# Kernel optimization log

Measured on AMD Instinct MI355X. Metric: run time of the kernel, lower is better.

The kernel has to match this reference:

```python
import jax, jax.numpy as jnp
import numpy as np

B, S, E = 2, 2048, 1024
H, HKV = 16, 4
D = E // H          # head_dim = 64
REP = H // HKV      # kv repeat factor = 4


def setup_inputs() -> dict:
    key = jax.random.key(0)
    ks = jax.random.split(key, 9)
    std = 0.02
    x = jax.random.normal(ks[0], (B, S, E), dtype=jnp.float32)
    # causal mask: True means masked (upper triangle, strictly above diagonal)
    mask = jnp.triu(jnp.ones((S, S), dtype=bool), k=1)
    wq_w = jax.random.normal(ks[1], (E, E), dtype=jnp.float32) * std
    wq_b = jax.random.normal(ks[2], (E,), dtype=jnp.float32) * std
    wk_w = jax.random.normal(ks[3], (HKV * D, E), dtype=jnp.float32) * std
    wk_b = jax.random.normal(ks[4], (HKV * D,), dtype=jnp.float32) * std
    wv_w = jax.random.normal(ks[5], (HKV * D, E), dtype=jnp.float32) * std
    wv_b = jax.random.normal(ks[6], (HKV * D,), dtype=jnp.float32) * std
    wo_w = jax.random.normal(ks[7], (E, E), dtype=jnp.float32) * std
    wo_b = jax.random.normal(ks[8], (E,), dtype=jnp.float32) * std
    return {"x": x, "mask": mask, "wq_w": wq_w, "wq_b": wq_b,
            "wk_w": wk_w, "wk_b": wk_b, "wv_w": wv_w, "wv_b": wv_b,
            "wo_w": wo_w, "wo_b": wo_b}


def reference(x, mask, wq_w, wq_b, wk_w, wk_b, wv_w, wv_b, wo_w, wo_b):
    b, s, e = x.shape
    # projections (torch Linear: x @ W.T + b)
    q = x @ wq_w.T + wq_b                       # [B,S,E]
    k = x @ wk_w.T + wk_b                       # [B,S,HKV*D]
    v = x @ wv_w.T + wv_b
    # q grouped by kv head: [B, HKV, REP, S, D]; k/v: [B, HKV, S, D]
    q = q.reshape(b, s, HKV, REP, D).transpose(0, 2, 3, 1, 4)
    k = k.reshape(b, s, HKV, D).transpose(0, 2, 1, 3)
    v = v.reshape(b, s, HKV, D).transpose(0, 2, 1, 3)
    scale = D ** (-0.5)
    # scores [B, HKV, REP, Sq, Skv] -- same math as physical repeat_kv
    scores = jnp.einsum('bgrsd,bgtd->bgrst', q, k) * scale
    scores = jnp.where(mask, -jnp.inf, scores)
    w = jax.nn.softmax(scores, axis=-1)
    ctx = jnp.einsum('bgrst,bgtd->bgrsd', w, v)  # [B,HKV,REP,S,D]
    ctx = ctx.transpose(0, 3, 1, 2, 4).reshape(b, s, e)
    return ctx @ wo_w.T + wo_b
```

## Files before the change

kernel.cpp:

```cpp
#include <hip/hip_runtime.h>


typedef __attribute__((ext_vector_type(8))) short bh8;
typedef __attribute__((ext_vector_type(4))) short sh4;
typedef __attribute__((ext_vector_type(4))) float fv4;
typedef __attribute__((ext_vector_type(2))) unsigned int uv2;

#define MFMA16 __builtin_amdgcn_mfma_f32_16x16x32_bf16

static __device__ __forceinline__ float fast_exp2(float x) {
  return __builtin_amdgcn_exp2f(x);
}
static __device__ __forceinline__ unsigned short f2bf(float f) {
  unsigned int u; __builtin_memcpy(&u, &f, 4);
  u += 0x7fffu + ((u >> 16) & 1u);
  return (unsigned short)(u >> 16);
}
static __device__ __forceinline__ unsigned int pack2(float a, float b) {
  return (unsigned int)(unsigned short)f2bf(a) |
         ((unsigned int)(unsigned short)f2bf(b) << 16);
}
static __device__ __forceinline__ void gload16(const short* g, short* l) {
  __builtin_amdgcn_global_load_lds(
      (const __attribute__((address_space(1))) void*)g,
      (__attribute__((address_space(3))) void*)l, 16, 0, 0);
}

static __device__ __forceinline__ bh8 pshuf(const float* p, int quad, int l16) {
  unsigned int u01 = pack2(p[0], p[1]);
  unsigned int u23 = pack2(p[2], p[3]);
  unsigned int u45 = pack2(p[4], p[5]);
  unsigned int u67 = pack2(p[6], p[7]);
  const int g0 = (((quad << 1)    ) & 3) * 16 + l16;
  const int g1 = (((quad << 1) + 1) & 3) * 16 + l16;
  unsigned int w0l = __shfl((int)u01, g0), w0h = __shfl((int)u45, g0);
  unsigned int w1l = __shfl((int)u23, g0), w1h = __shfl((int)u67, g0);
  unsigned int w2l = __shfl((int)u01, g1), w2h = __shfl((int)u45, g1);
  unsigned int w3l = __shfl((int)u23, g1), w3h = __shfl((int)u67, g1);
  const bool up = (quad & 2) != 0;
  union { unsigned int w[4]; bh8 v; } pu;
  pu.w[0] = up ? w0h : w0l;
  pu.w[1] = up ? w1h : w1l;
  pu.w[2] = up ? w2h : w2l;
  pu.w[3] = up ? w3h : w3l;
  return pu.v;
}

__global__ __launch_bounds__(256) void cvt_all(
    const float* __restrict__ x,  const float* __restrict__ wq,
    const float* __restrict__ wk, const float* __restrict__ wv,
    const float* __restrict__ wo,
    short* __restrict__ xb, short* __restrict__ wqkvb, short* __restrict__ wob)
{
  const int i = blockIdx.x * 256 + threadIdx.x;
  const float* src; short* dst; int j;
  if (i < 1048576)      { j = i;           src = x;  dst = xb; }
  else if (i < 1310720) { j = i - 1048576; src = wq; dst = wqkvb; }
  else if (i < 1376256) { j = i - 1310720; src = wk; dst = wqkvb + (size_t)1024 * 1024; }
  else if (i < 1441792) { j = i - 1376256; src = wv; dst = wqkvb + (size_t)1280 * 1024; }
  else                  { j = i - 1441792; src = wo; dst = wob; }
  const float4 v = ((const float4*)src)[j];
  sh4 o = { (short)f2bf(v.x), (short)f2bf(v.y),
            (short)f2bf(v.z), (short)f2bf(v.w) };
  ((sh4*)dst)[j] = o;
}

__global__ __launch_bounds__(256) void gemm_dbuf(
    const short* __restrict__ A, const short* __restrict__ W,
    const float* __restrict__ biasQ, const float* __restrict__ biasK,
    const float* __restrict__ biasV,
    short* __restrict__ Cq, short* __restrict__ Ck, short* __restrict__ Cvt,
    float* __restrict__ Cf,
    int M, int K, int S, int mode, float scaleQ)
{
  __shared__ short As[2][128 * 32];
  __shared__ short Bs[2][64 * 32];
  const int tid  = threadIdx.x;
  const int wave = tid >> 6, lane = tid & 63;
  const int quad = lane >> 4, l16 = lane & 15;
  const int row0 = blockIdx.x * 128, col0 = blockIdx.y * 64;
  const int wr = (wave >> 1) * 64, wc = (wave & 1) * 32;

  fv4 acc[4][2] = {};

  const int srow = wave * 16 + (lane >> 2);
  const int skp  = (lane & 3) * 8;
  const short* ag = A + (size_t)(row0 + srow) * K + skp;
  const short* bg = W + (size_t)(col0 + srow) * K + skp;

  auto stage = [&](int b, int k0) {
    gload16(ag + k0,                  &As[b][(wave * 16) * 32]);
    gload16(ag + (size_t)64 * K + k0, &As[b][(64 + wave * 16) * 32]);
    gload16(bg + k0,                  &Bs[b][(wave * 16) * 32]);
  };

  stage(0, 0);
  __syncthreads();
  const int nIter = K / 32;
  for (int it = 0; it < nIter; it++) {
    const int cur = it & 1;
    if (it + 1 < nIter) stage(cur ^ 1, (it + 1) * 32);

    bh8 af[4], bf[2];
    #pragma unroll
    for (int i = 0; i < 4; i++)
      af[i] = *(const bh8*)&As[cur][(wr + i * 16 + l16) * 32 + quad * 8];
    #pragma unroll
    for (int j = 0; j < 2; j++)
      bf[j] = *(const bh8*)&Bs[cur][(wc + j * 16 + l16) * 32 + quad * 8];
    #pragma unroll
    for (int i = 0; i < 4; i++)
      #pragma unroll
      for (int j = 0; j < 2; j++)
        acc[i][j] = MFMA16(af[i], bf[j], acc[i][j], 0, 0, 0);
    __syncthreads();
  }

  if (mode == 2) {
    float bv[2];
    #pragma unroll
    for (int j = 0; j < 2; j++) bv[j] = biasQ[col0 + wc + j * 16 + l16];
    #pragma unroll
    for (int i = 0; i < 4; i++) {
      const int row = row0 + wr + i * 16 + quad * 4;
      #pragma unroll
      for (int j = 0; j < 2; j++) {
        const int col = col0 + wc + j * 16 + l16;
        #pragma unroll
        for (int r = 0; r < 4; r++)
          Cf[(size_t)(row + r) * 1024 + col] = acc[i][j][r] + bv[j];
      }
    }
  } else if (col0 < 1024) {
    float bv[2];
    #pragma unroll
    for (int j = 0; j < 2; j++) bv[j] = biasQ[col0 + wc + j * 16 + l16];
    #pragma unroll
    for (int i = 0; i < 4; i++) {
      const int row = row0 + wr + i * 16 + quad * 4;
      #pragma unroll
      for (int j = 0; j < 2; j++) {
        const int col = col0 + wc + j * 16 + l16;
        #pragma unroll
        for (int r = 0; r < 4; r++)
          Cq[(size_t)(row + r) * 1024 + col] =
              (short)f2bf((acc[i][j][r] + bv[j]) * scaleQ);
      }
    }
  } else if (col0 < 1280) {
    float bv[2];
    #pragma unroll
    for (int j = 0; j < 2; j++) bv[j] = biasK[col0 + wc + j * 16 + l16 - 1024];
    #pragma unroll
    for (int i = 0; i < 4; i++) {
      const int row = row0 + wr + i * 16 + quad * 4;
      #pragma unroll
      for (int j = 0; j < 2; j++) {
        const int col = col0 + wc + j * 16 + l16 - 1024;
        #pragma unroll
        for (int r = 0; r < 4; r++)
          Ck[(size_t)(row + r) * 256 + col] = (short)f2bf(acc[i][j][r] + bv[j]);
      }
    }
  } else {
    float bv[2];
    #pragma unroll
    for (int j = 0; j < 2; j++) bv[j] = biasV[col0 + wc + j * 16 + l16 - 1280];
    const int b  = row0 / S;
    const int sb = row0 - b * S;
    #pragma unroll
    for (int i = 0; i < 4; i++) {
      const int s = sb + wr + i * 16 + quad * 4;
      #pragma unroll
      for (int j = 0; j < 2; j++) {
        const int np = col0 + wc + j * 16 + l16 - 1280;
        sh4 v = { (short)f2bf(acc[i][j][0] + bv[j]),
                  (short)f2bf(acc[i][j][1] + bv[j]),
                  (short)f2bf(acc[i][j][2] + bv[j]),
                  (short)f2bf(acc[i][j][3] + bv[j]) };
        *(sh4*)(Cvt + ((size_t)(b * 256 + np)) * S + s) = v;
      }
    }
  }
}

__global__ __launch_bounds__(256) void gqa_attn(
    const short* __restrict__ Q,
    const short* __restrict__ Kg,
    const short* __restrict__ Vt,
    short* __restrict__ ctx)
{
  const int S = 2048, E = 1024, KVE = 256;
  __shared__ short Ks[2][4096];
  __shared__ short Vs[2][4096];
  __shared__ short P2[4][16 * 72];

  const int wave = threadIdx.x >> 6;
  const int lane = threadIdx.x & 63;
  const int quad = lane >> 4, l16 = lane & 15;
  const int bh = blockIdx.y;
  const int b = bh >> 4, h = bh & 15, kv = h >> 2;

  const short* Kb = Kg + (size_t)b * S * KVE + kv * 64;
  const short* Vb = Vt + ((size_t)(b * 4 + kv)) * 64 * S;
  short* Pw = &P2[wave][0];

  const int srow = lane >> 3;
  const int scg  = (lane & 7) ^ srow;

  const int kc0 = (quad ^ (l16 & 7)) * 8;
  const int kc1 = ((quad ^ 4) ^ (l16 & 7)) * 8;
  const int pwr = l16 * 72;

  auto stageKV = [&](int buf, int t0) {
    #pragma unroll
    for (int e = 0; e < 2; e++) {
      const int g = wave * 2 + e;
      const int row = g * 8 + srow;
      gload16(Kb + (size_t)(t0 + row) * KVE + scg * 8, &Ks[buf][g * 512]);
      gload16(Vb + (size_t)row * S + t0 + scg * 8,     &Vs[buf][g * 512]);
    }
  };

  for (int ph = 0; ph < 2; ph++) {
    const int j = ph ? (31 - (int)blockIdx.x) : (int)blockIdx.x;
    const int qblk0 = j * 64;
    const int q0 = qblk0 + wave * 16;

    const short* qrow = Q + (size_t)(b * S + q0 + l16) * E + h * 64 + quad * 8;
    bh8 qf0 = *(const bh8*)(qrow);
    bh8 qf1 = *(const bh8*)(qrow + 32);

    fv4 acc0{}, acc1{}, acc2{}, acc3{};
    float rs = 0.f;

    const int nInt = qblk0 >> 6;
    if (nInt > 0) {
      stageKV(0, 0);
      __syncthreads();
      for (int it = 0; it < nInt; it++) {
        const int cur = it & 1;
        if (it + 1 < nInt) stageKV(cur ^ 1, (it + 1) * 64);

        fv4 st[4] = {};
        #pragma unroll
        for (int i = 0; i < 4; i++) {
          const int tb = (i * 16 + l16) * 64;
          bh8 k0 = *(const bh8*)&Ks[cur][tb + kc0];
          bh8 k1 = *(const bh8*)&Ks[cur][tb + kc1];
          st[i] = MFMA16(k0, qf0, st[i], 0, 0, 0);
          st[i] = MFMA16(k1, qf1, st[i], 0, 0, 0);
        }
        #pragma unroll
        for (int i = 0; i < 4; i++) {
          float p0 = fast_exp2(st[i][0]);
          float p1 = fast_exp2(st[i][1]);
          float p2 = fast_exp2(st[i][2]);
          float p3 = fast_exp2(st[i][3]);
          rs += (p0 + p1) + (p2 + p3);
          uv2 u = { pack2(p0, p1), pack2(p2, p3) };
          *(uv2*)&Pw[pwr + i * 16 + quad * 4] = u;
        }
        bh8 pfA = *(const bh8*)&Pw[pwr + quad * 8];
        bh8 pfB = *(const bh8*)&Pw[pwr + 32 + quad * 8];
        #pragma unroll
        for (int dt = 0; dt < 4; dt++) {
          const int db = (dt * 16 + l16) * 64;
          bh8 v0 = *(const bh8*)&Vs[cur][db + kc0];
          bh8 v1 = *(const bh8*)&Vs[cur][db + kc1];
          fv4* a = dt == 0 ? &acc0 : dt == 1 ? &acc1 : dt == 2 ? &acc2 : &acc3;
          *a = MFMA16(v0, pfA, *a, 0, 0, 0);
          *a = MFMA16(v1, pfB, *a, 0, 0, 0);
        }
        __syncthreads();
      }
    }

    const int nk = q0 + 16;
    for (int t0 = qblk0; t0 < nk; t0 += 32) {
      fv4 st0{}, st1{};
      {
        const short* kr = Kb + (size_t)(t0 + l16) * KVE + quad * 8;
        bh8 k0 = *(const bh8*)(kr);
        bh8 k1 = *(const bh8*)(kr + 32);
        st0 = MFMA16(k0, qf0, st0, 0, 0, 0);
        st0 = MFMA16(k1, qf1, st0, 0, 0, 0);
      }
      const bool do2 = (t0 + 16) < nk;
      if (do2) {
        const short* kr = Kb + (size_t)(t0 + 16 + l16) * KVE + quad * 8;
        bh8 k0 = *(const bh8*)(kr);
        bh8 k1 = *(const bh8*)(kr + 32);
        st1 = MFMA16(k0, qf0, st1, 0, 0, 0);
        st1 = MFMA16(k1, qf1, st1, 0, 0, 0);
      }
      const int qg = q0 + l16;
      float p[8];
      #pragma unroll
      for (int r = 0; r < 4; r++) {
        const int t = t0 + quad * 4 + r;
        p[r]     = (t <= qg)               ? fast_exp2(st0[r]) : 0.f;
        p[4 + r] = (do2 && (t + 16) <= qg) ? fast_exp2(st1[r]) : 0.f;
      }
      #pragma unroll
      for (int i = 0; i < 8; i++) rs += p[i];

      bh8 pf = pshuf(p, quad, l16);
      const short* vr = Vb + (size_t)l16 * S + t0 + quad * 8;
      acc0 = MFMA16(*(const bh8*)(vr),          pf, acc0, 0, 0, 0);
      acc1 = MFMA16(*(const bh8*)(vr + 16 * S), pf, acc1, 0, 0, 0);
      acc2 = MFMA16(*(const bh8*)(vr + 32 * S), pf, acc2, 0, 0, 0);
      acc3 = MFMA16(*(const bh8*)(vr + 48 * S), pf, acc3, 0, 0, 0);
    }

    float lsum = rs;
    lsum += __shfl_xor(lsum, 16);
    lsum += __shfl_xor(lsum, 32);
    const float inv = 1.f / lsum;

    short* orow = ctx + (size_t)(b * S + q0 + l16) * E + h * 64 + quad * 4;
    sh4 o0 = { (short)f2bf(acc0[0] * inv), (short)f2bf(acc0[1] * inv),
               (short)f2bf(acc0[2] * inv), (short)f2bf(acc0[3] * inv) };
    sh4 o1 = { (short)f2bf(acc1[0] * inv), (short)f2bf(acc1[1] * inv),
               (short)f2bf(acc1[2] * inv), (short)f2bf(acc1[3] * inv) };
    sh4 o2 = { (short)f2bf(acc2[0] * inv), (short)f2bf(acc2[1] * inv),
               (short)f2bf(acc2[2] * inv), (short)f2bf(acc2[3] * inv) };
    sh4 o3 = { (short)f2bf(acc3[0] * inv), (short)f2bf(acc3[1] * inv),
               (short)f2bf(acc3[2] * inv), (short)f2bf(acc3[3] * inv) };
    *(sh4*)(orow)      = o0;
    *(sh4*)(orow + 16) = o1;
    *(sh4*)(orow + 32) = o2;
    *(sh4*)(orow + 48) = o3;
  }
}

extern "C" void kernel_launch(void* const* d_in, const int* in_sizes, int n_in,
                              void* d_out, int out_size, void* d_ws, size_t ws_size,
                              hipStream_t stream)
{
  const float* x    = (const float*)d_in[0];
  const float* wq_w = (const float*)d_in[2];
  const float* wq_b = (const float*)d_in[3];
  const float* wk_w = (const float*)d_in[4];
  const float* wk_b = (const float*)d_in[5];
  const float* wv_w = (const float*)d_in[6];
  const float* wv_b = (const float*)d_in[7];
  const float* wo_w = (const float*)d_in[8];
  const float* wo_b = (const float*)d_in[9];
  float* out = (float*)d_out;

  const int S = 2048, E = 1024, M = 2 * S;
  const float sl2e = 0.125f * 1.44269504f;

  char* ob = (char*)d_out;
  short* Qb   = (short*)(ob);
  short* Kbuf = (short*)(ob + (size_t)( 8 << 20));
  short* Vtb  = (short*)(ob + (size_t)(10 << 20));

  char* ws = (char*)d_ws;
  short* xb    = (short*)(ws);
  short* wqkvb = (short*)(ws + (size_t)( 8 << 20));
  short* wob   = (short*)(ws + (size_t)(11 << 20));
  short* Cx    = xb;

  dim3 blk(256);
  cvt_all<<<dim3(6656), blk, 0, stream>>>(x, wq_w, wk_w, wv_w, wo_w,
                                          xb, wqkvb, wob);
  gemm_dbuf<<<dim3(M / 128, 1536 / 64), blk, 0, stream>>>(
      xb, wqkvb, wq_b, wk_b, wv_b, Qb, Kbuf, Vtb, nullptr, M, E, S, 0, sl2e);
  gqa_attn<<<dim3(16, 2 * 16), blk, 0, stream>>>(Qb, Kbuf, Vtb, Cx);
  gemm_dbuf<<<dim3(M / 128, 1024 / 64), blk, 0, stream>>>(
      Cx, wob, wo_b, nullptr, nullptr, nullptr, nullptr, nullptr, out,
      M, E, S, 2, 1.f);
}
```

Measured before the change: 181.0 us.

## Enlarge GEMM tiles to 128x128, split attention blocks, shuffle P in registers

The GEMM now uses 128x128 output tiles with a K-step of 64 and XOR-swizzled LDS in a single buffer. This raises data reuse per block but drops the double-buffered prefetch. The attention kernel no longer pairs a short and a long query block inside one workgroup; it launches one block per query tile with longest tiles first. The P matrix now goes to the PV MFMA through a register shuffle (pshuf) instead of a round trip through LDS. The trade-off is fewer GEMM blocks (more tail imbalance) and load latency that the single LDS buffer leaves exposed.

```diff
diff --git a/kernel.cpp b/kernel.cpp
--- a/kernel.cpp
+++ b/kernel.cpp
@@ -4,7 +4,6 @@
 typedef __attribute__((ext_vector_type(8))) short bh8;
 typedef __attribute__((ext_vector_type(4))) short sh4;
 typedef __attribute__((ext_vector_type(4))) float fv4;
-typedef __attribute__((ext_vector_type(2))) unsigned int uv2;
 
 #define MFMA16 __builtin_amdgcn_mfma_f32_16x16x32_bf16
 
@@ -65,7 +64,7 @@
   ((sh4*)dst)[j] = o;
 }
 
-__global__ __launch_bounds__(256) void gemm_dbuf(
+__global__ __launch_bounds__(256) void gemm_m97(
     const short* __restrict__ A, const short* __restrict__ W,
     const float* __restrict__ biasQ, const float* __restrict__ biasK,
     const float* __restrict__ biasV,
@@ -73,58 +72,58 @@
     float* __restrict__ Cf,
     int M, int K, int S, int mode, float scaleQ)
 {
-  __shared__ short As[2][128 * 32];
-  __shared__ short Bs[2][64 * 32];
-  const int tid  = threadIdx.x;
+  __shared__ short As[128 * 64];
+  __shared__ short Bs[128 * 64];
+  const int tid = threadIdx.x;
   const int wave = tid >> 6, lane = tid & 63;
   const int quad = lane >> 4, l16 = lane & 15;
-  const int row0 = blockIdx.x * 128, col0 = blockIdx.y * 64;
-  const int wr = (wave >> 1) * 64, wc = (wave & 1) * 32;
-
-  fv4 acc[4][2] = {};
-
-  const int srow = wave * 16 + (lane >> 2);
-  const int skp  = (lane & 3) * 8;
-  const short* ag = A + (size_t)(row0 + srow) * K + skp;
-  const short* bg = W + (size_t)(col0 + srow) * K + skp;
-
-  auto stage = [&](int b, int k0) {
-    gload16(ag + k0,                  &As[b][(wave * 16) * 32]);
-    gload16(ag + (size_t)64 * K + k0, &As[b][(64 + wave * 16) * 32]);
-    gload16(bg + k0,                  &Bs[b][(wave * 16) * 32]);
-  };
-
-  stage(0, 0);
-  __syncthreads();
-  const int nIter = K / 32;
-  for (int it = 0; it < nIter; it++) {
-    const int cur = it & 1;
-    if (it + 1 < nIter) stage(cur ^ 1, (it + 1) * 32);
-
-    bh8 af[4], bf[2];
-    #pragma unroll
-    for (int i = 0; i < 4; i++)
-      af[i] = *(const bh8*)&As[cur][(wr + i * 16 + l16) * 32 + quad * 8];
-    #pragma unroll
-    for (int j = 0; j < 2; j++)
-      bf[j] = *(const bh8*)&Bs[cur][(wc + j * 16 + l16) * 32 + quad * 8];
-    #pragma unroll
-    for (int i = 0; i < 4; i++)
-      #pragma unroll
-      for (int j = 0; j < 2; j++)
-        acc[i][j] = MFMA16(af[i], bf[j], acc[i][j], 0, 0, 0);
+  const int row0 = blockIdx.x * 128, col0 = blockIdx.y * 128;
+  const int wr = (wave >> 1) * 64, wc = (wave & 1) * 64;
+
+  fv4 acc[4][4] = {};
+
+  const int srow8  = lane >> 3;
+  const int schunk = (lane & 7) ^ srow8;
+  const short* agB = A + (size_t)(row0 + wave * 32 + srow8) * K + schunk * 8;
+  const short* bgB = W + (size_t)(col0 + wave * 32 + srow8) * K + schunk * 8;
+
+  const int fsw = (l16 & 7);
+
+  for (int k0 = 0; k0 < K; k0 += 64) {
     __syncthreads();
+    #pragma unroll
+    for (int g = 0; g < 4; g++) {
+      gload16(agB + (size_t)(g * 8) * K + k0, &As[(wave * 32 + g * 8) * 64]);
+      gload16(bgB + (size_t)(g * 8) * K + k0, &Bs[(wave * 32 + g * 8) * 64]);
+    }
+    __syncthreads();
+    #pragma unroll
+    for (int ks = 0; ks < 2; ks++) {
+      const int co = ((ks * 4 + quad) ^ fsw) * 8;
+      bh8 af[4], bf[4];
+      #pragma unroll
+      for (int i = 0; i < 4; i++)
+        af[i] = *(const bh8*)&As[(wr + i * 16 + l16) * 64 + co];
+      #pragma unroll
+      for (int j = 0; j < 4; j++)
+        bf[j] = *(const bh8*)&Bs[(wc + j * 16 + l16) * 64 + co];
+      #pragma unroll
+      for (int i = 0; i < 4; i++)
+        #pragma unroll
+        for (int j = 0; j < 4; j++)
+          acc[i][j] = MFMA16(af[i], bf[j], acc[i][j], 0, 0, 0);
+    }
   }
 
   if (mode == 2) {
-    float bv[2];
-    #pragma unroll
-    for (int j = 0; j < 2; j++) bv[j] = biasQ[col0 + wc + j * 16 + l16];
+    float bv[4];
+    #pragma unroll
+    for (int j = 0; j < 4; j++) bv[j] = biasQ[col0 + wc + j * 16 + l16];
     #pragma unroll
     for (int i = 0; i < 4; i++) {
       const int row = row0 + wr + i * 16 + quad * 4;
       #pragma unroll
-      for (int j = 0; j < 2; j++) {
+      for (int j = 0; j < 4; j++) {
         const int col = col0 + wc + j * 16 + l16;
         #pragma unroll
         for (int r = 0; r < 4; r++)
@@ -132,14 +131,14 @@
       }
     }
   } else if (col0 < 1024) {
-    float bv[2];
-    #pragma unroll
-    for (int j = 0; j < 2; j++) bv[j] = biasQ[col0 + wc + j * 16 + l16];
+    float bv[4];
+    #pragma unroll
+    for (int j = 0; j < 4; j++) bv[j] = biasQ[col0 + wc + j * 16 + l16];
     #pragma unroll
     for (int i = 0; i < 4; i++) {
       const int row = row0 + wr + i * 16 + quad * 4;
       #pragma unroll
-      for (int j = 0; j < 2; j++) {
+      for (int j = 0; j < 4; j++) {
         const int col = col0 + wc + j * 16 + l16;
         #pragma unroll
         for (int r = 0; r < 4; r++)
@@ -148,14 +147,14 @@
       }
     }
   } else if (col0 < 1280) {
-    float bv[2];
-    #pragma unroll
-    for (int j = 0; j < 2; j++) bv[j] = biasK[col0 + wc + j * 16 + l16 - 1024];
+    float bv[4];
+    #pragma unroll
+    for (int j = 0; j < 4; j++) bv[j] = biasK[col0 + wc + j * 16 + l16 - 1024];
     #pragma unroll
     for (int i = 0; i < 4; i++) {
       const int row = row0 + wr + i * 16 + quad * 4;
       #pragma unroll
-      for (int j = 0; j < 2; j++) {
+      for (int j = 0; j < 4; j++) {
         const int col = col0 + wc + j * 16 + l16 - 1024;
         #pragma unroll
         for (int r = 0; r < 4; r++)
@@ -163,16 +162,16 @@
       }
     }
   } else {
-    float bv[2];
-    #pragma unroll
-    for (int j = 0; j < 2; j++) bv[j] = biasV[col0 + wc + j * 16 + l16 - 1280];
+    float bv[4];
+    #pragma unroll
+    for (int j = 0; j < 4; j++) bv[j] = biasV[col0 + wc + j * 16 + l16 - 1280];
     const int b  = row0 / S;
     const int sb = row0 - b * S;
     #pragma unroll
     for (int i = 0; i < 4; i++) {
       const int s = sb + wr + i * 16 + quad * 4;
       #pragma unroll
-      for (int j = 0; j < 2; j++) {
+      for (int j = 0; j < 4; j++) {
         const int np = col0 + wc + j * 16 + l16 - 1280;
         sh4 v = { (short)f2bf(acc[i][j][0] + bv[j]),
                   (short)f2bf(acc[i][j][1] + bv[j]),
@@ -193,24 +192,23 @@
   const int S = 2048, E = 1024, KVE = 256;
   __shared__ short Ks[2][4096];
   __shared__ short Vs[2][4096];
-  __shared__ short P2[4][16 * 72];
 
   const int wave = threadIdx.x >> 6;
   const int lane = threadIdx.x & 63;
   const int quad = lane >> 4, l16 = lane & 15;
   const int bh = blockIdx.y;
   const int b = bh >> 4, h = bh & 15, kv = h >> 2;
+  const int j = 31 - (int)blockIdx.x;
+  const int qblk0 = j * 64;
+  const int q0 = qblk0 + wave * 16;
 
   const short* Kb = Kg + (size_t)b * S * KVE + kv * 64;
   const short* Vb = Vt + ((size_t)(b * 4 + kv)) * 64 * S;
-  short* Pw = &P2[wave][0];
 
   const int srow = lane >> 3;
   const int scg  = (lane & 7) ^ srow;
-
   const int kc0 = (quad ^ (l16 & 7)) * 8;
   const int kc1 = ((quad ^ 4) ^ (l16 & 7)) * 8;
-  const int pwr = l16 * 72;
 
   auto stageKV = [&](int buf, int t0) {
     #pragma unroll
@@ -222,116 +220,111 @@
     }
   };
 
-  for (int ph = 0; ph < 2; ph++) {
-    const int j = ph ? (31 - (int)blockIdx.x) : (int)blockIdx.x;
-    const int qblk0 = j * 64;
-    const int q0 = qblk0 + wave * 16;
-
-    const short* qrow = Q + (size_t)(b * S + q0 + l16) * E + h * 64 + quad * 8;
-    bh8 qf0 = *(const bh8*)(qrow);
-    bh8 qf1 = *(const bh8*)(qrow + 32);
-
-    fv4 acc0{}, acc1{}, acc2{}, acc3{};
-    float rs = 0.f;
-
-    const int nInt = qblk0 >> 6;
-    if (nInt > 0) {
-      stageKV(0, 0);
+  const short* qrow = Q + (size_t)(b * S + q0 + l16) * E + h * 64 + quad * 8;
+  bh8 qf0 = *(const bh8*)(qrow);
+  bh8 qf1 = *(const bh8*)(qrow + 32);
+
+  fv4 acc0{}, acc1{}, acc2{}, acc3{};
+  float rs = 0.f;
+
+  const int nInt = j;
+  if (nInt > 0) {
+    stageKV(0, 0);
+    __syncthreads();
+    for (int it = 0; it < nInt; it++) {
+      const int cur = it & 1;
+      if (it + 1 < nInt) stageKV(cur ^ 1, (it + 1) * 64);
+
+      fv4 st[4] = {};
+      #pragma unroll
+      for (int i = 0; i < 4; i++) {
+        const int tb = (i * 16 + l16) * 64;
+        bh8 k0 = *(const bh8*)&Ks[cur][tb + kc0];
+        bh8 k1 = *(const bh8*)&Ks[cur][tb + kc1];
+        st[i] = MFMA16(k0, qf0, st[i], 0, 0, 0);
+        st[i] = MFMA16(k1, qf1, st[i], 0, 0, 0);
+      }
+      float p[16];
+      #pragma unroll
+      for (int i = 0; i < 4; i++) {
+        p[i * 4 + 0] = fast_exp2(st[i][0]);
+        p[i * 4 + 1] = fast_exp2(st[i][1]);
+        p[i * 4 + 2] = fast_exp2(st[i][2]);
+        p[i * 4 + 3] = fast_exp2(st[i][3]);
+      }
+      #pragma unroll
+      for (int i = 0; i < 16; i++) rs += p[i];
+
+      bh8 pfA = pshuf(p,     quad, l16);
+      bh8 pfB = pshuf(p + 8, quad, l16);
+      #pragma unroll
+      for (int dt = 0; dt < 4; dt++) {
+        const int db = (dt * 16 + l16) * 64;
+        bh8 v0 = *(const bh8*)&Vs[cur][db + kc0];
+        bh8 v1 = *(const bh8*)&Vs[cur][db + kc1];
+        fv4* a = dt == 0 ? &acc0 : dt == 1 ? &acc1 : dt == 2 ? &acc2 : &acc3;
+        *a = MFMA16(v0, pfA, *a, 0, 0, 0);
+        *a = MFMA16(v1, pfB, *a, 0, 0, 0);
+      }
       __syncthreads();
-      for (int it = 0; it < nInt; it++) {
-        const int cur = it & 1;
-        if (it + 1 < nInt) stageKV(cur ^ 1, (it + 1) * 64);
-
-        fv4 st[4] = {};
-        #pragma unroll
-        for (int i = 0; i < 4; i++) {
-          const int tb = (i * 16 + l16) * 64;
-          bh8 k0 = *(const bh8*)&Ks[cur][tb + kc0];
-          bh8 k1 = *(const bh8*)&Ks[cur][tb + kc1];
-          st[i] = MFMA16(k0, qf0, st[i], 0, 0, 0);
-          st[i] = MFMA16(k1, qf1, st[i], 0, 0, 0);
-        }
-        #pragma unroll
-        for (int i = 0; i < 4; i++) {
-          float p0 = fast_exp2(st[i][0]);
-          float p1 = fast_exp2(st[i][1]);
-          float p2 = fast_exp2(st[i][2]);
-          float p3 = fast_exp2(st[i][3]);
-          rs += (p0 + p1) + (p2 + p3);
-          uv2 u = { pack2(p0, p1), pack2(p2, p3) };
-          *(uv2*)&Pw[pwr + i * 16 + quad * 4] = u;
-        }
-        bh8 pfA = *(const bh8*)&Pw[pwr + quad * 8];
-        bh8 pfB = *(const bh8*)&Pw[pwr + 32 + quad * 8];
-        #pragma unroll
-        for (int dt = 0; dt < 4; dt++) {
-          const int db = (dt * 16 + l16) * 64;
-          bh8 v0 = *(const bh8*)&Vs[cur][db + kc0];
-          bh8 v1 = *(const bh8*)&Vs[cur][db + kc1];
-          fv4* a = dt == 0 ? &acc0 : dt == 1 ? &acc1 : dt == 2 ? &acc2 : &acc3;
-          *a = MFMA16(v0, pfA, *a, 0, 0, 0);
-          *a = MFMA16(v1, pfB, *a, 0, 0, 0);
-        }
-        __syncthreads();
-      }
-    }
-
-    const int nk = q0 + 16;
-    for (int t0 = qblk0; t0 < nk; t0 += 32) {
-      fv4 st0{}, st1{};
-      {
-        const short* kr = Kb + (size_t)(t0 + l16) * KVE + quad * 8;
-        bh8 k0 = *(const bh8*)(kr);
-        bh8 k1 = *(const bh8*)(kr + 32);
-        st0 = MFMA16(k0, qf0, st0, 0, 0, 0);
-        st0 = MFMA16(k1, qf1, st0, 0, 0, 0);
-      }
-      const bool do2 = (t0 + 16) < nk;
-      if (do2) {
-        const short* kr = Kb + (size_t)(t0 + 16 + l16) * KVE + quad * 8;
-        bh8 k0 = *(const bh8*)(kr);
-        bh8 k1 = *(const bh8*)(kr + 32);
-        st1 = MFMA16(k0, qf0, st1, 0, 0, 0);
-        st1 = MFMA16(k1, qf1, st1, 0, 0, 0);
-      }
-      const int qg = q0 + l16;
-      float p[8];
-      #pragma unroll
-      for (int r = 0; r < 4; r++) {
-        const int t = t0 + quad * 4 + r;
-        p[r]     = (t <= qg)               ? fast_exp2(st0[r]) : 0.f;
-        p[4 + r] = (do2 && (t + 16) <= qg) ? fast_exp2(st1[r]) : 0.f;
-      }
-      #pragma unroll
-      for (int i = 0; i < 8; i++) rs += p[i];
-
-      bh8 pf = pshuf(p, quad, l16);
-      const short* vr = Vb + (size_t)l16 * S + t0 + quad * 8;
-      acc0 = MFMA16(*(const bh8*)(vr),          pf, acc0, 0, 0, 0);
-      acc1 = MFMA16(*(const bh8*)(vr + 16 * S), pf, acc1, 0, 0, 0);
-      acc2 = MFMA16(*(const bh8*)(vr + 32 * S), pf, acc2, 0, 0, 0);
-      acc3 = MFMA16(*(const bh8*)(vr + 48 * S), pf, acc3, 0, 0, 0);
-    }
-
-    float lsum = rs;
-    lsum += __shfl_xor(lsum, 16);
-    lsum += __shfl_xor(lsum, 32);
-    const float inv = 1.f / lsum;
-
-    short* orow = ctx + (size_t)(b * S + q0 + l16) * E + h * 64 + quad * 4;
-    sh4 o0 = { (short)f2bf(acc0[0] * inv), (short)f2bf(acc0[1] * inv),
-               (short)f2bf(acc0[2] * inv), (short)f2bf(acc0[3] * inv) };
-    sh4 o1 = { (short)f2bf(acc1[0] * inv), (short)f2bf(acc1[1] * inv),
-               (short)f2bf(acc1[2] * inv), (short)f2bf(acc1[3] * inv) };
-    sh4 o2 = { (short)f2bf(acc2[0] * inv), (short)f2bf(acc2[1] * inv),
-               (short)f2bf(acc2[2] * inv), (short)f2bf(acc2[3] * inv) };
-    sh4 o3 = { (short)f2bf(acc3[0] * inv), (short)f2bf(acc3[1] * inv),
-               (short)f2bf(acc3[2] * inv), (short)f2bf(acc3[3] * inv) };
-    *(sh4*)(orow)      = o0;
-    *(sh4*)(orow + 16) = o1;
-    *(sh4*)(orow + 32) = o2;
-    *(sh4*)(orow + 48) = o3;
+    }
   }
+
+  const int nk = q0 + 16;
+  for (int t0 = qblk0; t0 < nk; t0 += 32) {
+    fv4 st0{}, st1{};
+    {
+      const short* kr = Kb + (size_t)(t0 + l16) * KVE + quad * 8;
+      bh8 k0 = *(const bh8*)(kr);
+      bh8 k1 = *(const bh8*)(kr + 32);
+      st0 = MFMA16(k0, qf0, st0, 0, 0, 0);
+      st0 = MFMA16(k1, qf1, st0, 0, 0, 0);
+    }
+    const bool do2 = (t0 + 16) < nk;
+    if (do2) {
+      const short* kr = Kb + (size_t)(t0 + 16 + l16) * KVE + quad * 8;
+      bh8 k0 = *(const bh8*)(kr);
+      bh8 k1 = *(const bh8*)(kr + 32);
+      st1 = MFMA16(k0, qf0, st1, 0, 0, 0);
+      st1 = MFMA16(k1, qf1, st1, 0, 0, 0);
+    }
+    const int qg = q0 + l16;
+    float p[8];
+    #pragma unroll
+    for (int r = 0; r < 4; r++) {
+      const int t = t0 + quad * 4 + r;
+      p[r]     = (t <= qg)               ? fast_exp2(st0[r]) : 0.f;
+      p[4 + r] = (do2 && (t + 16) <= qg) ? fast_exp2(st1[r]) : 0.f;
+    }
+    #pragma unroll
+    for (int i = 0; i < 8; i++) rs += p[i];
+
+    bh8 pf = pshuf(p, quad, l16);
+    const short* vr = Vb + (size_t)l16 * S + t0 + quad * 8;
+    acc0 = MFMA16(*(const bh8*)(vr),          pf, acc0, 0, 0, 0);
+    acc1 = MFMA16(*(const bh8*)(vr + 16 * S), pf, acc1, 0, 0, 0);
+    acc2 = MFMA16(*(const bh8*)(vr + 32 * S), pf, acc2, 0, 0, 0);
+    acc3 = MFMA16(*(const bh8*)(vr + 48 * S), pf, acc3, 0, 0, 0);
+  }
+
+  float lsum = rs;
+  lsum += __shfl_xor(lsum, 16);
+  lsum += __shfl_xor(lsum, 32);
+  const float inv = 1.f / lsum;
+
+  short* orow = ctx + (size_t)(b * S + q0 + l16) * E + h * 64 + quad * 4;
+  sh4 o0 = { (short)f2bf(acc0[0] * inv), (short)f2bf(acc0[1] * inv),
+             (short)f2bf(acc0[2] * inv), (short)f2bf(acc0[3] * inv) };
+  sh4 o1 = { (short)f2bf(acc1[0] * inv), (short)f2bf(acc1[1] * inv),
+             (short)f2bf(acc1[2] * inv), (short)f2bf(acc1[3] * inv) };
+  sh4 o2 = { (short)f2bf(acc2[0] * inv), (short)f2bf(acc2[1] * inv),
+             (short)f2bf(acc2[2] * inv), (short)f2bf(acc2[3] * inv) };
+  sh4 o3 = { (short)f2bf(acc3[0] * inv), (short)f2bf(acc3[1] * inv),
+             (short)f2bf(acc3[2] * inv), (short)f2bf(acc3[3] * inv) };
+  *(sh4*)(orow)      = o0;
+  *(sh4*)(orow + 16) = o1;
+  *(sh4*)(orow + 32) = o2;
+  *(sh4*)(orow + 48) = o3;
 }
 
 extern "C" void kernel_launch(void* const* d_in, const int* in_sizes, int n_in,
@@ -366,10 +359,10 @@
   dim3 blk(256);
   cvt_all<<<dim3(6656), blk, 0, stream>>>(x, wq_w, wk_w, wv_w, wo_w,
                                           xb, wqkvb, wob);
-  gemm_dbuf<<<dim3(M / 128, 1536 / 64), blk, 0, stream>>>(
+  gemm_m97<<<dim3(M / 128, 1536 / 128), blk, 0, stream>>>(
       xb, wqkvb, wq_b, wk_b, wv_b, Qb, Kbuf, Vtb, nullptr, M, E, S, 0, sl2e);
-  gqa_attn<<<dim3(16, 2 * 16), blk, 0, stream>>>(Qb, Kbuf, Vtb, Cx);
-  gemm_dbuf<<<dim3(M / 128, 1024 / 64), blk, 0, stream>>>(
+  gqa_attn<<<dim3(32, 2 * 16), blk, 0, stream>>>(Qb, Kbuf, Vtb, Cx);
+  gemm_m97<<<dim3(M / 128, 1024 / 128), blk, 0, stream>>>(
       Cx, wob, wo_b, nullptr, nullptr, nullptr, nullptr, nullptr, out,
       M, E, S, 2, 1.f);
 }
```

After: 206.6 us. 1.14x slower.
